# Kernel optimization log

Hardware: AMD Instinct MI355X
Metric: run time of the kernel (lower is better)

## Reference

```python
import jax, jax.numpy as jnp
import numpy as np

DIM = 768
NUM_HEADS = 12
HEAD_DIM = DIM // NUM_HEADS
SCALE = HEAD_DIM ** -0.5


def setup_inputs() -> dict:
    key = jax.random.key(0)
    k1, k2, k3 = jax.random.split(key, 3)
    x = jax.random.normal(k1, (32, 577, DIM), dtype=jnp.float32)
    # torch nn.Linear weights are [out_features, in_features]
    W_qkv = jax.random.normal(k2, (3 * DIM, DIM), dtype=jnp.float32) * (DIM ** -0.5)
    W_proj = jax.random.normal(k3, (DIM, DIM), dtype=jnp.float32) * (DIM ** -0.5)
    b_proj = jnp.zeros((DIM,), dtype=jnp.float32)
    return {"x": x, "W_qkv": W_qkv, "W_proj": W_proj, "b_proj": b_proj}


def reference(x, W_qkv, W_proj, b_proj):
    B, N, C = x.shape
    H, D = NUM_HEADS, C // NUM_HEADS
    # qkv: [B, N, 3C] -> [3, B, H, N, D]
    qkv = (x @ W_qkv.T).reshape(B, N, 3, H, D).transpose(2, 0, 3, 1, 4)
    q, k, v = qkv[0], qkv[1], qkv[2]
    attn = jnp.einsum('bhnd,bhmd->bhnm', q, k) * SCALE
    attn = jax.nn.softmax(attn, axis=-1)
    out = jnp.einsum('bhnm,bhmd->bhnd', attn, v)  # [B, H, N, D]
    out = out.transpose(0, 2, 1, 3).reshape(B, N, C)
    return out @ W_proj.T + b_proj
```

## Files before the change

kernel.cpp:

```cpp
#include <hip/hip_runtime.h>
#include <math.h>

#define SEQ    577
#define BATCH  32
#define DIM    768
#define NHEAD  12
#define HDIM   64
#define MROWS  (BATCH * SEQ)
#define QKVN   (3 * DIM)

using half4   = __attribute__((ext_vector_type(4))) _Float16;
using half8   = __attribute__((ext_vector_type(8))) _Float16;
using floatx4 = __attribute__((ext_vector_type(4))) float;

typedef __attribute__((address_space(1))) const unsigned int GU;
typedef __attribute__((address_space(3))) unsigned int LU;

__device__ __forceinline__ void gld_lds16(const _Float16* g, _Float16* l) {
    __builtin_amdgcn_global_load_lds((const GU*)g, (LU*)l, 16, 0, 0);
}

__global__ void cvt_f32_f16(const float* __restrict__ in,
                            _Float16* __restrict__ out, int n4)
{
    int i = blockIdx.x * blockDim.x + threadIdx.x;
    int stride = gridDim.x * blockDim.x;
    for (; i < n4; i += stride) {
        float4 v = ((const float4*)in)[i];
        half4 h;
        h[0] = (_Float16)v.x; h[1] = (_Float16)v.y;
        h[2] = (_Float16)v.z; h[3] = (_Float16)v.w;
        ((half4*)out)[i] = h;
    }
}

template<int OUT_HALF, int HAS_BIAS>
__global__ __launch_bounds__(256) void gemm_f16_lds(
    const _Float16* __restrict__ A, const _Float16* __restrict__ B,
    const float* __restrict__ bias, void* __restrict__ Cp,
    int M, int N, int K, int npm, int npn)
{
    __shared__ _Float16 As[128 * 32];
    __shared__ _Float16 Bs[128 * 32];

    const int GROUP = 8;
    int pid  = blockIdx.x;
    int ngrp = GROUP * npn;
    int g    = pid / ngrp;
    int fm   = g * GROUP;
    int gm   = npm - fm; if (gm > GROUP) gm = GROUP;
    int pm   = fm + (pid % ngrp) % gm;
    int pn   = (pid % ngrp) / gm;
    const int m0 = pm * 128, n0 = pn * 128;

    const int t    = threadIdx.x, lane = t & 63, wv = t >> 6;
    const int quad = lane >> 4,   ln   = lane & 15;
    const int wm   = wv >> 1,     wn   = wv & 1;

    floatx4 acc[4][4];
#pragma unroll
    for (int mt = 0; mt < 4; mt++)
#pragma unroll
        for (int nt = 0; nt < 4; nt++) acc[mt][nt] = {0.f, 0.f, 0.f, 0.f};

    const int sr = wv * 32 + (lane >> 2);
    const int sc = (lane & 3) * 8;
    int ma0 = m0 + sr;      if (ma0 > M - 1) ma0 = M - 1;
    int ma1 = m0 + sr + 16; if (ma1 > M - 1) ma1 = M - 1;
    const _Float16* Ag0 = A + (size_t)ma0 * K + sc;
    const _Float16* Ag1 = A + (size_t)ma1 * K + sc;
    const _Float16* Bg0 = B + (size_t)(n0 + sr) * K + sc;
    const _Float16* Bg1 = B + (size_t)(n0 + sr + 16) * K + sc;
    _Float16* Al0 = &As[sr * 32 + sc];
    _Float16* Al1 = &As[(sr + 16) * 32 + sc];
    _Float16* Bl0 = &Bs[sr * 32 + sc];
    _Float16* Bl1 = &Bs[(sr + 16) * 32 + sc];

    for (int k0 = 0; k0 < K; k0 += 32) {
        __syncthreads();
        gld_lds16(Ag0 + k0, Al0);
        gld_lds16(Ag1 + k0, Al1);
        gld_lds16(Bg0 + k0, Bl0);
        gld_lds16(Bg1 + k0, Bl1);
        __syncthreads();

        half8 af[4], bf[4];
#pragma unroll
        for (int mt = 0; mt < 4; mt++)
            af[mt] = *(const half8*)&As[(wm * 64 + mt * 16 + ln) * 32 + quad * 8];
#pragma unroll
        for (int nt = 0; nt < 4; nt++)
            bf[nt] = *(const half8*)&Bs[(wn * 64 + nt * 16 + ln) * 32 + quad * 8];
#pragma unroll
        for (int mt = 0; mt < 4; mt++)
#pragma unroll
            for (int nt = 0; nt < 4; nt++)
                acc[mt][nt] = __builtin_amdgcn_mfma_f32_16x16x32_f16(
                    af[mt], bf[nt], acc[mt][nt], 0, 0, 0);
    }

    float bv[4];
    if constexpr (HAS_BIAS) {
#pragma unroll
        for (int nt = 0; nt < 4; nt++) bv[nt] = bias[n0 + wn * 64 + nt * 16 + ln];
    }
    float*    C32 = (float*)Cp;
    _Float16* C16 = (_Float16*)Cp;
#pragma unroll
    for (int mt = 0; mt < 4; mt++)
#pragma unroll
        for (int r = 0; r < 4; r++) {
            int m = m0 + wm * 64 + mt * 16 + quad * 4 + r;
            if (m < M) {
#pragma unroll
                for (int nt = 0; nt < 4; nt++) {
                    int col = n0 + wn * 64 + nt * 16 + ln;
                    float v = acc[mt][nt][r];
                    if constexpr (HAS_BIAS) v += bv[nt];
                    if constexpr (OUT_HALF) C16[(size_t)m * N + col] = (_Float16)v;
                    else                    C32[(size_t)m * N + col] = v;
                }
            }
        }
}

__global__ __launch_bounds__(256) void attn_f16(
    const _Float16* __restrict__ qkv, _Float16* __restrict__ outp)
{
    constexpr int LQ = 72;
    constexpr int LV = 68;
    __shared__ _Float16 Qs[64 * LQ];
    __shared__ _Float16 Ks[64 * LQ];
    __shared__ _Float16 Vs[64 * LV];

    const int t    = threadIdx.x, lane = t & 63, wv = t >> 6;
    const int quad = lane >> 4,   ln   = lane & 15;
    const int q0   = blockIdx.x * 64;
    const int hd   = blockIdx.y, b = blockIdx.z;
    const _Float16* base = qkv + (size_t)b * SEQ * QKVN;

#pragma unroll
    for (int i = 0; i < 2; i++) {
        int f = t + (i << 8);
        int row = f >> 3, c = f & 7;
        int n = q0 + row; if (n >= SEQ) n = SEQ - 1;
        *(uint4*)&Qs[row * LQ + c * 8] =
            *(const uint4*)(base + (size_t)n * QKVN + hd * HDIM + c * 8);
    }

    float mrun = -3e38f, lrun = 0.f;
    floatx4 o[4];
#pragma unroll
    for (int dt = 0; dt < 4; dt++) o[dt] = {0.f, 0.f, 0.f, 0.f};

    for (int kt0 = 0; kt0 < 10; kt0++) {
        const int k0 = kt0 * 64;

        uint4 kreg[2];
#pragma unroll
        for (int i = 0; i < 2; i++) {
            int f = t + (i << 8);
            int row = f >> 3, c = f & 7;
            int n = k0 + row; if (n >= SEQ) n = SEQ - 1;
            kreg[i] = *(const uint4*)(base + (size_t)n * QKVN + DIM + hd * HDIM + c * 8);
        }
        unsigned short vreg[16];
        const int vd = lane;
#pragma unroll
        for (int i = 0; i < 16; i++) {
            int key = wv + i * 4;
            int n = k0 + key; if (n >= SEQ) n = SEQ - 1;
            vreg[i] = *(const unsigned short*)(base + (size_t)n * QKVN + 2 * DIM + hd * HDIM + vd);
        }

        __syncthreads();
#pragma unroll
        for (int i = 0; i < 2; i++) {
            int f = t + (i << 8);
            int row = f >> 3, c = f & 7;
            *(uint4*)&Ks[row * LQ + c * 8] = kreg[i];
        }
        {
            unsigned short* vs = (unsigned short*)Vs;
#pragma unroll
            for (int i = 0; i < 16; i++)
                vs[vd * LV + (wv + i * 4)] = vreg[i];
        }
        __syncthreads();

        floatx4 sacc[4];
#pragma unroll
        for (int mt = 0; mt < 4; mt++) sacc[mt] = {0.f, 0.f, 0.f, 0.f};
#pragma unroll
        for (int kd = 0; kd < 4; kd++) {
            half4 qf = *(const half4*)&Qs[(wv * 16 + ln) * LQ + kd * 16 + quad * 4];
#pragma unroll
            for (int mt = 0; mt < 4; mt++) {
                half4 kf = *(const half4*)&Ks[(mt * 16 + ln) * LQ + kd * 16 + quad * 4];
                sacc[mt] = __builtin_amdgcn_mfma_f32_16x16x16f16(kf, qf, sacc[mt], 0, 0, 0);
            }
        }

        float sv[4][4];
        float tmax = -3e38f;
#pragma unroll
        for (int mt = 0; mt < 4; mt++)
#pragma unroll
            for (int r = 0; r < 4; r++) {
                float v = sacc[mt][r] * 0.125f;
                if (k0 + mt * 16 + quad * 4 + r >= SEQ) v = -3e38f;
                sv[mt][r] = v;
                tmax = fmaxf(tmax, v);
            }
        tmax = fmaxf(tmax, __shfl_xor(tmax, 16));
        tmax = fmaxf(tmax, __shfl_xor(tmax, 32));
        float mnew  = fmaxf(mrun, tmax);
        float alpha = __expf(mrun - mnew);
        float lsum  = 0.f;
        half4 pf[4];
#pragma unroll
        for (int mt = 0; mt < 4; mt++)
#pragma unroll
            for (int r = 0; r < 4; r++) {
                float p = __expf(sv[mt][r] - mnew);
                lsum += p;
                pf[mt][r] = (_Float16)p;
            }
        lsum += __shfl_xor(lsum, 16);
        lsum += __shfl_xor(lsum, 32);
        lrun = lrun * alpha + lsum;
        mrun = mnew;

#pragma unroll
        for (int dt = 0; dt < 4; dt++) {
            o[dt][0] *= alpha; o[dt][1] *= alpha;
            o[dt][2] *= alpha; o[dt][3] *= alpha;
        }

#pragma unroll
        for (int kt = 0; kt < 4; kt++)
#pragma unroll
            for (int dt = 0; dt < 4; dt++) {
                half4 vf = *(const half4*)&Vs[(dt * 16 + ln) * LV + kt * 16 + quad * 4];
                o[dt] = __builtin_amdgcn_mfma_f32_16x16x16f16(vf, pf[kt], o[dt], 0, 0, 0);
            }
    }

    const int q = q0 + wv * 16 + ln;
    if (q < SEQ) {
        float linv = 1.f / lrun;
#pragma unroll
        for (int dt = 0; dt < 4; dt++) {
            half4 hv;
            hv[0] = (_Float16)(o[dt][0] * linv);
            hv[1] = (_Float16)(o[dt][1] * linv);
            hv[2] = (_Float16)(o[dt][2] * linv);
            hv[3] = (_Float16)(o[dt][3] * linv);
            *(half4*)&outp[(size_t)(b * SEQ + q) * DIM + hd * HDIM + dt * 16 + quad * 4] = hv;
        }
    }
}

extern "C" void kernel_launch(void* const* d_in, const int* in_sizes, int n_in,
                              void* d_out, int out_size, void* d_ws, size_t ws_size,
                              hipStream_t stream)
{
    const float* x     = (const float*)d_in[0];
    const float* Wqkv  = (const float*)d_in[1];
    const float* Wproj = (const float*)d_in[2];
    const float* bproj = (const float*)d_in[3];
    float* out = (float*)d_out;

    const size_t NX = (size_t)MROWS * DIM;
    const size_t NWQ = (size_t)QKVN * DIM;
    const size_t NWP = (size_t)DIM * DIM;

    _Float16* x16    = (_Float16*)d_ws;
    _Float16* Wq16   = x16 + NX;
    _Float16* Wp16   = Wq16 + NWQ;
    _Float16* qkv16  = Wp16 + NWP;
    _Float16* attn16 = qkv16 + (size_t)MROWS * QKVN;

    cvt_f32_f16<<<2048, 256, 0, stream>>>(x, x16, (int)(NX / 4));
    cvt_f32_f16<<<1024, 256, 0, stream>>>(Wqkv, Wq16, (int)(NWQ / 4));
    cvt_f32_f16<<<576, 256, 0, stream>>>(Wproj, Wp16, (int)(NWP / 4));

    {
        int npm = (MROWS + 127) / 128, npn = QKVN / 128;
        gemm_f16_lds<1, 0><<<npm * npn, 256, 0, stream>>>(
            x16, Wq16, nullptr, qkv16, MROWS, QKVN, DIM, npm, npn);
    }

    attn_f16<<<dim3((SEQ + 63) / 64, NHEAD, BATCH), 256, 0, stream>>>(qkv16, attn16);

    {
        int npm = (MROWS + 127) / 128, npn = DIM / 128;
        gemm_f16_lds<0, 1><<<npm * npn, 256, 0, stream>>>(
            attn16, Wp16, bproj, out, MROWS, DIM, DIM, npm, npn);
    }
}
```

Measured before the change: 411.9 us.

## Process 128 queries per attention block with register Q and 16x16x32 MFMA

```diff
diff --git a/kernel.cpp b/kernel.cpp
--- a/kernel.cpp
+++ b/kernel.cpp
@@ -20,17 +20,23 @@
     __builtin_amdgcn_global_load_lds((const GU*)g, (LU*)l, 16, 0, 0);
 }
 
-__global__ void cvt_f32_f16(const float* __restrict__ in,
-                            _Float16* __restrict__ out, int n4)
+__global__ void cvt3_f32_f16(const float* __restrict__ a, _Float16* __restrict__ ao, int na4,
+                             const float* __restrict__ b, _Float16* __restrict__ bo, int nb4,
+                             const float* __restrict__ c, _Float16* __restrict__ co, int nc4)
 {
     int i = blockIdx.x * blockDim.x + threadIdx.x;
     int stride = gridDim.x * blockDim.x;
-    for (; i < n4; i += stride) {
-        float4 v = ((const float4*)in)[i];
+    int total = na4 + nb4 + nc4;
+    for (; i < total; i += stride) {
+        const float4* src; half4* dst; int j = i;
+        if (j < na4)            { src = (const float4*)a; dst = (half4*)ao; }
+        else if ((j -= na4) < nb4) { src = (const float4*)b; dst = (half4*)bo; }
+        else { j -= nb4;          src = (const float4*)c; dst = (half4*)co; }
+        float4 v = src[j];
         half4 h;
         h[0] = (_Float16)v.x; h[1] = (_Float16)v.y;
         h[2] = (_Float16)v.z; h[3] = (_Float16)v.w;
-        ((half4*)out)[i] = h;
+        dst[j] = h;
     }
 }
 
@@ -127,114 +133,120 @@
 __global__ __launch_bounds__(256) void attn_f16(
     const _Float16* __restrict__ qkv, _Float16* __restrict__ outp)
 {
-    constexpr int LQ = 72;
-    constexpr int LV = 68;
-    __shared__ _Float16 Qs[64 * LQ];
-    __shared__ _Float16 Ks[64 * LQ];
+    constexpr int LK = 72, LV = 68;
+    __shared__ _Float16 Ks[64 * LK];
     __shared__ _Float16 Vs[64 * LV];
 
     const int t    = threadIdx.x, lane = t & 63, wv = t >> 6;
     const int quad = lane >> 4,   ln   = lane & 15;
-    const int q0   = blockIdx.x * 64;
-    const int hd   = blockIdx.y, b = blockIdx.z;
+    const int q0   = blockIdx.x * 128;
+    const int hd   = blockIdx.y,  b    = blockIdx.z;
     const _Float16* base = qkv + (size_t)b * SEQ * QKVN;
 
-#pragma unroll
-    for (int i = 0; i < 2; i++) {
-        int f = t + (i << 8);
-        int row = f >> 3, c = f & 7;
-        int n = q0 + row; if (n >= SEQ) n = SEQ - 1;
-        *(uint4*)&Qs[row * LQ + c * 8] =
-            *(const uint4*)(base + (size_t)n * QKVN + hd * HDIM + c * 8);
-    }
-
-    float mrun = -3e38f, lrun = 0.f;
-    floatx4 o[4];
-#pragma unroll
-    for (int dt = 0; dt < 4; dt++) o[dt] = {0.f, 0.f, 0.f, 0.f};
+    half8 qreg[2][2];
+#pragma unroll
+    for (int qc = 0; qc < 2; qc++) {
+        int q = q0 + wv * 32 + qc * 16 + ln; if (q >= SEQ) q = SEQ - 1;
+#pragma unroll
+        for (int kd = 0; kd < 2; kd++)
+            qreg[qc][kd] = *(const half8*)(base + (size_t)q * QKVN + hd * HDIM + kd * 32 + quad * 8);
+    }
+
+    const float CL = 0.125f * 1.44269504f;
+    float m2[2] = {-3e38f, -3e38f};
+    float lr[2] = {0.f, 0.f};
+    floatx4 o[2][4];
+#pragma unroll
+    for (int qc = 0; qc < 2; qc++)
+#pragma unroll
+        for (int dt = 0; dt < 4; dt++) o[qc][dt] = {0.f, 0.f, 0.f, 0.f};
 
     for (int kt0 = 0; kt0 < 10; kt0++) {
         const int k0 = kt0 * 64;
 
-        uint4 kreg[2];
+        uint4 krg[2], vrg[2];
 #pragma unroll
         for (int i = 0; i < 2; i++) {
-            int f = t + (i << 8);
-            int row = f >> 3, c = f & 7;
-            int n = k0 + row; if (n >= SEQ) n = SEQ - 1;
-            kreg[i] = *(const uint4*)(base + (size_t)n * QKVN + DIM + hd * HDIM + c * 8);
-        }
-        unsigned short vreg[16];
-        const int vd = lane;
-#pragma unroll
-        for (int i = 0; i < 16; i++) {
-            int key = wv + i * 4;
+            int idx = t + (i << 8);
+            int key = idx >> 3, dc = idx & 7;
             int n = k0 + key; if (n >= SEQ) n = SEQ - 1;
-            vreg[i] = *(const unsigned short*)(base + (size_t)n * QKVN + 2 * DIM + hd * HDIM + vd);
-        }
-
+            const _Float16* p = base + (size_t)n * QKVN + DIM + hd * HDIM + dc * 8;
+            krg[i] = *(const uint4*)p;
+            vrg[i] = *(const uint4*)(p + DIM);
+        }
         __syncthreads();
 #pragma unroll
         for (int i = 0; i < 2; i++) {
-            int f = t + (i << 8);
-            int row = f >> 3, c = f & 7;
-            *(uint4*)&Ks[row * LQ + c * 8] = kreg[i];
-        }
-        {
+            int idx = t + (i << 8);
+            int key = idx >> 3, dc = idx & 7;
+            *(uint4*)&Ks[key * LK + dc * 8] = krg[i];
+            const unsigned short* vh = (const unsigned short*)&vrg[i];
             unsigned short* vs = (unsigned short*)Vs;
 #pragma unroll
-            for (int i = 0; i < 16; i++)
-                vs[vd * LV + (wv + i * 4)] = vreg[i];
+            for (int j = 0; j < 8; j++)
+                vs[(dc * 8 + j) * LV + key] = vh[j];
         }
         __syncthreads();
 
-        floatx4 sacc[4];
-#pragma unroll
-        for (int mt = 0; mt < 4; mt++) sacc[mt] = {0.f, 0.f, 0.f, 0.f};
-#pragma unroll
-        for (int kd = 0; kd < 4; kd++) {
-            half4 qf = *(const half4*)&Qs[(wv * 16 + ln) * LQ + kd * 16 + quad * 4];
+        floatx4 sacc[2][4];
+#pragma unroll
+        for (int qc = 0; qc < 2; qc++)
+#pragma unroll
+            for (int mt = 0; mt < 4; mt++) sacc[qc][mt] = {0.f, 0.f, 0.f, 0.f};
+#pragma unroll
+        for (int kd = 0; kd < 2; kd++) {
+            half8 kf[4];
+#pragma unroll
+            for (int mt = 0; mt < 4; mt++)
+                kf[mt] = *(const half8*)&Ks[(mt * 16 + ln) * LK + kd * 32 + quad * 8];
 #pragma unroll
             for (int mt = 0; mt < 4; mt++) {
-                half4 kf = *(const half4*)&Ks[(mt * 16 + ln) * LQ + kd * 16 + quad * 4];
-                sacc[mt] = __builtin_amdgcn_mfma_f32_16x16x16f16(kf, qf, sacc[mt], 0, 0, 0);
-            }
-        }
-
-        float sv[4][4];
-        float tmax = -3e38f;
-#pragma unroll
-        for (int mt = 0; mt < 4; mt++)
-#pragma unroll
-            for (int r = 0; r < 4; r++) {
-                float v = sacc[mt][r] * 0.125f;
-                if (k0 + mt * 16 + quad * 4 + r >= SEQ) v = -3e38f;
-                sv[mt][r] = v;
-                tmax = fmaxf(tmax, v);
-            }
-        tmax = fmaxf(tmax, __shfl_xor(tmax, 16));
-        tmax = fmaxf(tmax, __shfl_xor(tmax, 32));
-        float mnew  = fmaxf(mrun, tmax);
-        float alpha = __expf(mrun - mnew);
-        float lsum  = 0.f;
-        half4 pf[4];
-#pragma unroll
-        for (int mt = 0; mt < 4; mt++)
-#pragma unroll
-            for (int r = 0; r < 4; r++) {
-                float p = __expf(sv[mt][r] - mnew);
-                lsum += p;
-                pf[mt][r] = (_Float16)p;
-            }
-        lsum += __shfl_xor(lsum, 16);
-        lsum += __shfl_xor(lsum, 32);
-        lrun = lrun * alpha + lsum;
-        mrun = mnew;
-
-#pragma unroll
-        for (int dt = 0; dt < 4; dt++) {
-            o[dt][0] *= alpha; o[dt][1] *= alpha;
-            o[dt][2] *= alpha; o[dt][3] *= alpha;
+                sacc[0][mt] = __builtin_amdgcn_mfma_f32_16x16x32_f16(kf[mt], qreg[0][kd], sacc[0][mt], 0, 0, 0);
+                sacc[1][mt] = __builtin_amdgcn_mfma_f32_16x16x32_f16(kf[mt], qreg[1][kd], sacc[1][mt], 0, 0, 0);
+            }
+        }
+
+        if (k0 + 64 > SEQ) {
+#pragma unroll
+            for (int mt = 0; mt < 4; mt++)
+#pragma unroll
+                for (int r = 0; r < 4; r++)
+                    if (k0 + mt * 16 + quad * 4 + r >= SEQ) {
+                        sacc[0][mt][r] = -3e38f;
+                        sacc[1][mt][r] = -3e38f;
+                    }
+        }
+
+        half4 pf[2][4];
+#pragma unroll
+        for (int qc = 0; qc < 2; qc++) {
+            float tm = -3e38f;
+#pragma unroll
+            for (int mt = 0; mt < 4; mt++)
+#pragma unroll
+                for (int r = 0; r < 4; r++) tm = fmaxf(tm, sacc[qc][mt][r]);
+            tm = fmaxf(tm, __shfl_xor(tm, 16));
+            tm = fmaxf(tm, __shfl_xor(tm, 32));
+            float m2n = fmaxf(m2[qc], tm * CL);
+            float al  = exp2f(m2[qc] - m2n);
+            float ls  = 0.f;
+#pragma unroll
+            for (int mt = 0; mt < 4; mt++)
+#pragma unroll
+                for (int r = 0; r < 4; r++) {
+                    float p = exp2f(fmaf(sacc[qc][mt][r], CL, -m2n));
+                    ls += p;
+                    pf[qc][mt][r] = (_Float16)p;
+                }
+            ls += __shfl_xor(ls, 16);
+            ls += __shfl_xor(ls, 32);
+            lr[qc] = lr[qc] * al + ls;
+            m2[qc] = m2n;
+#pragma unroll
+            for (int dt = 0; dt < 4; dt++) {
+                o[qc][dt][0] *= al; o[qc][dt][1] *= al;
+                o[qc][dt][2] *= al; o[qc][dt][3] *= al;
+            }
         }
 
 #pragma unroll
@@ -242,21 +254,25 @@
 #pragma unroll
             for (int dt = 0; dt < 4; dt++) {
                 half4 vf = *(const half4*)&Vs[(dt * 16 + ln) * LV + kt * 16 + quad * 4];
-                o[dt] = __builtin_amdgcn_mfma_f32_16x16x16f16(vf, pf[kt], o[dt], 0, 0, 0);
-            }
-    }
-
-    const int q = q0 + wv * 16 + ln;
-    if (q < SEQ) {
-        float linv = 1.f / lrun;
-#pragma unroll
-        for (int dt = 0; dt < 4; dt++) {
-            half4 hv;
-            hv[0] = (_Float16)(o[dt][0] * linv);
-            hv[1] = (_Float16)(o[dt][1] * linv);
-            hv[2] = (_Float16)(o[dt][2] * linv);
-            hv[3] = (_Float16)(o[dt][3] * linv);
-            *(half4*)&outp[(size_t)(b * SEQ + q) * DIM + hd * HDIM + dt * 16 + quad * 4] = hv;
+                o[0][dt] = __builtin_amdgcn_mfma_f32_16x16x16f16(vf, pf[0][kt], o[0][dt], 0, 0, 0);
+                o[1][dt] = __builtin_amdgcn_mfma_f32_16x16x16f16(vf, pf[1][kt], o[1][dt], 0, 0, 0);
+            }
+    }
+
+#pragma unroll
+    for (int qc = 0; qc < 2; qc++) {
+        int q = q0 + wv * 32 + qc * 16 + ln;
+        if (q < SEQ) {
+            float inv = 1.f / lr[qc];
+#pragma unroll
+            for (int dt = 0; dt < 4; dt++) {
+                half4 hv;
+                hv[0] = (_Float16)(o[qc][dt][0] * inv);
+                hv[1] = (_Float16)(o[qc][dt][1] * inv);
+                hv[2] = (_Float16)(o[qc][dt][2] * inv);
+                hv[3] = (_Float16)(o[qc][dt][3] * inv);
+                *(half4*)&outp[(size_t)(b * SEQ + q) * DIM + hd * HDIM + dt * 16 + quad * 4] = hv;
+            }
         }
     }
 }
@@ -271,7 +287,7 @@
     const float* bproj = (const float*)d_in[3];
     float* out = (float*)d_out;
 
-    const size_t NX = (size_t)MROWS * DIM;
+    const size_t NX  = (size_t)MROWS * DIM;
     const size_t NWQ = (size_t)QKVN * DIM;
     const size_t NWP = (size_t)DIM * DIM;
 
@@ -281,9 +297,9 @@
     _Float16* qkv16  = Wp16 + NWP;
     _Float16* attn16 = qkv16 + (size_t)MROWS * QKVN;
 
-    cvt_f32_f16<<<2048, 256, 0, stream>>>(x, x16, (int)(NX / 4));
-    cvt_f32_f16<<<1024, 256, 0, stream>>>(Wqkv, Wq16, (int)(NWQ / 4));
-    cvt_f32_f16<<<576, 256, 0, stream>>>(Wproj, Wp16, (int)(NWP / 4));
+    cvt3_f32_f16<<<2048, 256, 0, stream>>>(x, x16, (int)(NX / 4),
+                                           Wqkv, Wq16, (int)(NWQ / 4),
+                                           Wproj, Wp16, (int)(NWP / 4));
 
     {
         int npm = (MROWS + 127) / 128, npn = QKVN / 128;
@@ -291,7 +307,7 @@
             x16, Wq16, nullptr, qkv16, MROWS, QKVN, DIM, npm, npn);
     }
 
-    attn_f16<<<dim3((SEQ + 63) / 64, NHEAD, BATCH), 256, 0, stream>>>(qkv16, attn16);
+    attn_f16<<<dim3((SEQ + 127) / 128, NHEAD, BATCH), 256, 0, stream>>>(qkv16, attn16);
 
     {
         int npm = (MROWS + 127) / 128, npn = DIM / 128;
```

Result: faster. 384.2 us (-6.7%).
